# Optimization experiments

Hardware: AMD Instinct MI355X
Metric: run time of the kernel (lower is better)

Reference implementation:

```python
import jax, jax.numpy as jnp
import numpy as np

# Fixed module configuration (matches init_kwargs)
B, T, H, W, C = 2, 16, 32, 32, 512
NH, DH = 8, 64          # num_heads, head_dim = C // NH
MLP = 2048
EPS = 1e-6              # flax LayerNorm default epsilon


def _xavier(key, shape):
    fan_in, fan_out = shape[-2], shape[-1]
    lim = np.sqrt(6.0 / (fan_in + fan_out)).astype(np.float32)
    return jax.random.uniform(key, shape, jnp.float32, -lim, lim)


def setup_inputs() -> dict:
    key = jax.random.key(0)
    ks = jax.random.split(key, 8)
    return {
        "x": jax.random.normal(ks[0], (B, T * H * W, C), jnp.float32),
        # per-axis (stacked: 0=time, 1=height, 2=width) attention params
        "ln_scale": jnp.ones((3, C), jnp.float32),
        "ln_bias": jnp.zeros((3, C), jnp.float32),
        "wq": _xavier(ks[1], (3, C, C)), "bq": jnp.zeros((3, C), jnp.float32),
        "wk": _xavier(ks[2], (3, C, C)), "bk": jnp.zeros((3, C), jnp.float32),
        "wv": _xavier(ks[3], (3, C, C)), "bv": jnp.zeros((3, C), jnp.float32),
        "wo": _xavier(ks[4], (3, C, C)), "bo": jnp.zeros((3, C), jnp.float32),
        # final LN + MLP params
        "ln_mlp_scale": jnp.ones((C,), jnp.float32),
        "ln_mlp_bias": jnp.zeros((C,), jnp.float32),
        "w1": _xavier(ks[5], (C, MLP)),
        "b1": jax.random.normal(ks[6], (MLP,), jnp.float32) * 1e-6,
        "w2": _xavier(ks[7], (MLP, C)),
        "b2": jnp.zeros((C,), jnp.float32),
    }


def _ln(x, scale, bias):
    m = jnp.mean(x, axis=-1, keepdims=True)
    v = jnp.var(x, axis=-1, keepdims=True)
    return (x - m) * jax.lax.rsqrt(v + EPS) * scale + bias


def _mha(x, wq, bq, wk, bk, wv, bv, wo, bo):
    # x: [Bf, S, C]; standard flax-style MHA (query scaled by 1/sqrt(head_dim))
    Bf, S, _ = x.shape
    q = (x @ wq + bq).reshape(Bf, S, NH, DH) * (1.0 / np.sqrt(DH).astype(np.float32))
    k = (x @ wk + bk).reshape(Bf, S, NH, DH)
    v = (x @ wv + bv).reshape(Bf, S, NH, DH)
    a = jax.nn.softmax(jnp.einsum('bqhd,bkhd->bhqk', q, k), axis=-1)
    o = jnp.einsum('bhqk,bkhd->bqhd', a, v).reshape(Bf, S, C)
    return o @ wo + bo


def _axial(x5, axis, sc, bi, wq, bq, wk, bk, wv, bv, wo, bo):
    # fold all non-`axis` spatial dims into batch, attend along `axis`
    other = [a for a in (1, 2, 3) if a != axis]
    perm = [0] + other + [axis, 4]
    xp = jnp.transpose(x5, perm)                      # [..., S_axis, C]
    pshape = xp.shape
    x1 = xp.reshape(-1, pshape[-2], C)                # [Bf, S_axis, C]
    y = _mha(_ln(x1, sc, bi), wq, bq, wk, bk, wv, bv, wo, bo) + x1  # pre-LN residual
    y = y.reshape(pshape)
    inv = list(np.argsort(perm))
    return jnp.transpose(y, inv)


def reference(x, ln_scale, ln_bias, wq, bq, wk, bk, wv, bv, wo, bo,
              ln_mlp_scale, ln_mlp_bias, w1, b1, w2, b2):
    x5 = x.reshape(B, T, H, W, C)
    for i, axis in enumerate((1, 2, 3)):  # time, height, width
        x5 = _axial(x5, axis, ln_scale[i], ln_bias[i], wq[i], bq[i],
                    wk[i], bk[i], wv[i], bv[i], wo[i], bo[i])
    xf = x5.reshape(B, T * H * W, C)
    y = _ln(xf, ln_mlp_scale, ln_mlp_bias)
    y = jax.nn.gelu(y @ w1 + b1) @ w2 + b2            # gelu approximate=True (flax default)
    return xf + y
```

## Files before the change

### kernel.cpp

```cpp
#include <hip/hip_runtime.h>
#include <hip/hip_bf16.h>

typedef __attribute__((ext_vector_type(8))) short short8;
typedef __attribute__((ext_vector_type(4))) float f32x4;

static __device__ __forceinline__ short f2bf(float f) {
    union { __hip_bfloat16 h; short s; } u;
    u.h = __float2bfloat16(f);
    return u.s;
}

static __device__ __forceinline__ float gelu_tanh(float v) {
    const float c = 0.7978845608028654f;
    float t = tanhf(c * (v + 0.044715f * v * v * v));
    return 0.5f * v * (1.f + t);
}

static __device__ __forceinline__ void gload16(const void* g, void* l) {
    __builtin_amdgcn_global_load_lds(
        (const __attribute__((address_space(1))) void*)g,
        (__attribute__((address_space(3))) void*)l, 16, 0, 0);
}

__global__ __launch_bounds__(256) void cvt_weights(
    const float* __restrict__ wq, const float* __restrict__ wk,
    const float* __restrict__ wv, const float* __restrict__ wo,
    const float* __restrict__ w1, const float* __restrict__ w2,
    short* __restrict__ wT)
{
    const long NSQ = 12L * 262144;
    long gid = (long)blockIdx.x * 256 + threadIdx.x;
    if (gid < NSQ) {
        int m = (int)(gid >> 18);
        int rem = (int)(gid & 262143);
        int n = rem >> 9, k = rem & 511;
        int a = m >> 2, t = m & 3;
        const float* src = (t == 0) ? wq : (t == 1) ? wk : (t == 2) ? wv : wo;
        wT[gid] = f2bf(src[(long)a * 262144 + (long)k * 512 + n]);
    } else if (gid < NSQ + 1048576) {
        int r = (int)(gid - NSQ);
        int n = r >> 9, k = r & 511;
        wT[gid] = f2bf(w1[(long)k * 2048 + n]);
    } else {
        int r = (int)(gid - NSQ - 1048576);
        int n = r >> 11, k = r & 2047;
        wT[gid] = f2bf(w2[(long)k * 512 + n]);
    }
}

__global__ __launch_bounds__(256) void ln_kernel(
    const float* __restrict__ x, const float* __restrict__ sc,
    const float* __restrict__ bi, short* __restrict__ out)
{
    int row = blockIdx.x * 4 + (threadIdx.x >> 6);
    int lane = threadIdx.x & 63;
    const float* xr = x + (long)row * 512 + lane * 8;
    f32x4 v0 = *(const f32x4*)xr;
    f32x4 v1 = *(const f32x4*)(xr + 4);
    float s = 0.f, ss = 0.f;
#pragma unroll
    for (int i = 0; i < 4; i++) { s += v0[i] + v1[i]; ss += v0[i] * v0[i] + v1[i] * v1[i]; }
#pragma unroll
    for (int m = 1; m < 64; m <<= 1) { s += __shfl_xor(s, m, 64); ss += __shfl_xor(ss, m, 64); }
    float mean = s * (1.f / 512.f);
    float var  = ss * (1.f / 512.f) - mean * mean;
    float rs = rsqrtf(var + 1e-6f);
    f32x4 s0 = *(const f32x4*)(sc + lane * 8);
    f32x4 s1 = *(const f32x4*)(sc + lane * 8 + 4);
    f32x4 b0 = *(const f32x4*)(bi + lane * 8);
    f32x4 b1 = *(const f32x4*)(bi + lane * 8 + 4);
    short8 o;
#pragma unroll
    for (int i = 0; i < 4; i++) o[i]     = f2bf((v0[i] - mean) * rs * s0[i] + b0[i]);
#pragma unroll
    for (int i = 0; i < 4; i++) o[4 + i] = f2bf((v1[i] - mean) * rs * s1[i] + b1[i]);
    *(short8*)(out + (long)row * 512 + lane * 8) = o;
}

template<int EPI>
__global__ __launch_bounds__(256, 2) void gemm_nt(
    const short* __restrict__ A, const short* __restrict__ Bt,
    const float* __restrict__ bias, const float* __restrict__ bias2,
    const float* __restrict__ bias3,
    const float* __restrict__ res, float* __restrict__ outf,
    short* __restrict__ outb, int M, int N, int K, float scale)
{
    __shared__ __align__(16) short AB[2][2][8192];
    const int t = threadIdx.x;
    const int lane = t & 63, wid = t >> 6;
    const int wm = wid >> 1, wn = wid & 1;
    const int m0 = blockIdx.x * 128, n0 = blockIdx.y * 128;

    const short* Ag = A  + (long)m0 * K;
    const short* Bg = Bt + (long)n0 * K;

    f32x4 acc[4][4];
#pragma unroll
    for (int i = 0; i < 4; i++)
#pragma unroll
        for (int j = 0; j < 4; j++) acc[i][j] = (f32x4){0.f, 0.f, 0.f, 0.f};

    const long rowOff = (long)(t >> 3) * K + (t & 7) * 8;
    const int  ldsOff = t * 16;
    char* const lbase = (char*)AB;
    const int NT = K >> 6;

#pragma unroll
    for (int c = 0; c < 4; c++) {
        gload16(Ag + rowOff + (long)c * 32 * K, lbase + c * 4096 + ldsOff);
        gload16(Bg + rowOff + (long)c * 32 * K, lbase + 16384 + c * 4096 + ldsOff);
    }

    int cur = 0;
    for (int tt = 0; tt < NT; ++tt) {
        if (tt + 1 < NT) {
            const short* Asrc = Ag + (tt + 1) * 64 + rowOff;
            const short* Bsrc = Bg + (tt + 1) * 64 + rowOff;
            char* dst = lbase + (cur ^ 1) * 32768;
#pragma unroll
            for (int c = 0; c < 4; c++) {
                gload16(Asrc + (long)c * 32 * K, dst + c * 4096 + ldsOff);
                gload16(Bsrc + (long)c * 32 * K, dst + 16384 + c * 4096 + ldsOff);
            }
            asm volatile("s_waitcnt vmcnt(8)" ::: "memory");
        } else {
            asm volatile("s_waitcnt vmcnt(0)" ::: "memory");
        }
        asm volatile("s_barrier" ::: "memory");

        const char* rb = lbase + cur * 32768;
        const int arow = wm * 64 + (lane & 15);
        const int brow = wn * 64 + (lane & 15);
        const int kb = (lane >> 4) * 16;
#pragma unroll
        for (int ks = 0; ks < 2; ++ks) {
            short8 af[4], bfr[4];
#pragma unroll
            for (int f = 0; f < 4; f++) {
                af[f]  = *(short8*)(rb + (arow + f * 16) * 128 + kb + ks * 64);
                bfr[f] = *(short8*)(rb + 16384 + (brow + f * 16) * 128 + kb + ks * 64);
            }
#pragma unroll
            for (int i = 0; i < 4; i++)
#pragma unroll
                for (int j = 0; j < 4; j++)
                    acc[i][j] = __builtin_amdgcn_mfma_f32_16x16x32_bf16(af[i], bfr[j], acc[i][j], 0, 0, 0);
        }
        asm volatile("s_barrier" ::: "memory");
        cur ^= 1;
    }

    if (EPI == 1) {
#pragma unroll
        for (int j = 0; j < 4; j++) {
            int col = n0 + wn * 64 + j * 16 + (lane & 15);
            float bv = bias[col];
#pragma unroll
            for (int i = 0; i < 4; i++) {
                int row0 = m0 + wm * 64 + i * 16 + ((lane >> 4) << 2);
#pragma unroll
                for (int r = 0; r < 4; r++) {
                    long idx = (long)(row0 + r) * N + col;
                    outf[idx] = acc[i][j][r] + bv + res[idx];
                }
            }
        }
    } else {
        float* sl = (float*)((char*)AB + (wid >> 1) * 32768 + (wid & 1) * 8192);
        const int r0g = m0 + wm * 64;
        const int c0g = n0 + wn * 64;
#pragma unroll
        for (int half = 0; half < 2; ++half) {
#pragma unroll
            for (int jj = 0; jj < 2; ++jj) {
                int j = half * 2 + jj;
                int col = c0g + j * 16 + (lane & 15);
                float bv, sc_part = 1.f;
                if (EPI == 3) {
                    int part = col >> 9;
                    const float* bp = (part == 0) ? bias : (part == 1) ? bias2 : bias3;
                    bv = bp[col & 511];
                    if (part == 0) sc_part = scale;
                } else {
                    bv = bias[col];
                }
#pragma unroll
                for (int i = 0; i < 4; i++)
#pragma unroll
                    for (int r = 0; r < 4; r++) {
                        int rl = i * 16 + ((lane >> 4) << 2) + r;
                        int cl = jj * 16 + (lane & 15);
                        float v = (acc[i][j][r] + bv) * sc_part;
                        if (EPI == 2) v = gelu_tanh(v);
                        sl[(rl * 32 + cl) ^ ((rl & 7) << 2)] = v;
                    }
            }
            __syncthreads();
#pragma unroll
            for (int s = 0; s < 4; s++) {
                int rl = s * 16 + (lane >> 2);
                int fb = rl * 32 + (lane & 3) * 8;
                int sw = (rl & 7) << 2;
                f32x4 lo = *(f32x4*)&sl[fb ^ sw];
                f32x4 hi = *(f32x4*)&sl[(fb + 4) ^ sw];
                short8 o;
#pragma unroll
                for (int e = 0; e < 4; e++) { o[e] = f2bf(lo[e]); o[4 + e] = f2bf(hi[e]); }
                *(short8*)(outb + (long)(r0g + rl) * N + c0g + half * 32 + (lane & 3) * 8) = o;
            }
            if (half == 0) __syncthreads();
        }
    }
}

template<int S, int PASS>
__global__ __launch_bounds__(64) void attn_kernel(
    const short* __restrict__ Q, const short* __restrict__ Kx,
    const short* __restrict__ V, short* __restrict__ O, int ld)
{
    constexpr int MF = S / 16;
    constexpr int SP = 32;
    __shared__ __align__(16) short P_lds[S * SP];
    __shared__ __align__(16) short Vt[64 * SP];

    const int lane = threadIdx.x;
    const int pair = blockIdx.x;
    const int head = pair & 7;
    const int bf = pair >> 3;
    long base; int stride;
    if (PASS == 0)      { base = (long)(bf >> 10) * 16384 + (bf & 1023); stride = 1024; }
    else if (PASS == 1) { int b = bf >> 9, t = (bf >> 5) & 15, w = bf & 31; base = (long)b * 16384 + t * 1024 + w; stride = 32; }
    else                { int b = bf >> 9, t = (bf >> 5) & 15, h = bf & 31; base = (long)b * 16384 + t * 1024 + (h << 5); stride = 1; }
    const int hoff = head * 64;

    if (S == 16) {
        short8 z = {0, 0, 0, 0, 0, 0, 0, 0};
        *(short8*)(P_lds + lane * 8) = z;
#pragma unroll
        for (int i = 0; i < 4; i++) *(short8*)(Vt + lane * 32 + i * 8) = z;
        __syncthreads();
    }

    short8 qf[MF][2], kf[MF][2];
#pragma unroll
    for (int f = 0; f < MF; f++) {
        int r = f * 16 + (lane & 15);
        const short* qp = Q + (base + (long)r * stride) * ld + hoff + ((lane >> 4) * 8);
        qf[f][0] = *(const short8*)qp;
        qf[f][1] = *(const short8*)(qp + 32);
        const short* kp = Kx + (base + (long)r * stride) * ld + hoff + ((lane >> 4) * 8);
        kf[f][0] = *(const short8*)kp;
        kf[f][1] = *(const short8*)(kp + 32);
    }

    short8 vv[4];
    const int vr  = (S == 32) ? (lane & 31) : (lane & 15);
    const int vd0 = (S == 32) ? ((lane >> 5) * 32) : ((lane >> 4) * 16);
    constexpr int NVC = (S == 32) ? 4 : 2;
    {
        const short* vp = V + (base + (long)vr * stride) * ld + hoff + vd0;
#pragma unroll
        for (int c = 0; c < NVC; c++) vv[c] = *(const short8*)(vp + c * 8);
    }
#pragma unroll
    for (int c = 0; c < NVC; c++)
#pragma unroll
        for (int e = 0; e < 8; e++)
            Vt[(vd0 + c * 8 + e) * SP + vr] = vv[c][e];

    f32x4 zero4 = {0.f, 0.f, 0.f, 0.f};
    f32x4 sc[MF][MF];
#pragma unroll
    for (int i = 0; i < MF; i++)
#pragma unroll
        for (int j = 0; j < MF; j++) {
            f32x4 a = __builtin_amdgcn_mfma_f32_16x16x32_bf16(qf[i][0], kf[j][0], zero4, 0, 0, 0);
            sc[i][j] = __builtin_amdgcn_mfma_f32_16x16x32_bf16(qf[i][1], kf[j][1], a, 0, 0, 0);
        }

#pragma unroll
    for (int i = 0; i < MF; i++) {
#pragma unroll
        for (int r = 0; r < 4; r++) {
            float mx = sc[i][0][r];
            if (MF == 2) mx = fmaxf(mx, sc[i][1][r]);
#pragma unroll
            for (int m = 1; m < 16; m <<= 1) mx = fmaxf(mx, __shfl_xor(mx, m, 64));
            float e0 = expf(sc[i][0][r] - mx);
            float e1 = (MF == 2) ? expf(sc[i][1][r] - mx) : 0.f;
            float sum = e0 + e1;
#pragma unroll
            for (int m = 1; m < 16; m <<= 1) sum += __shfl_xor(sum, m, 64);
            float inv = 1.f / sum;
            int row = i * 16 + ((lane >> 4) << 2) + r;
            P_lds[row * SP + (lane & 15)] = f2bf(e0 * inv);
            if (MF == 2) P_lds[row * SP + 16 + (lane & 15)] = f2bf(e1 * inv);
        }
    }
    __syncthreads();

    short8 pa[MF];
#pragma unroll
    for (int f = 0; f < MF; f++)
        pa[f] = *(const short8*)(P_lds + (f * 16 + (lane & 15)) * SP + (lane >> 4) * 8);
    short8 vbf[4];
#pragma unroll
    for (int n = 0; n < 4; n++)
        vbf[n] = *(const short8*)(Vt + (n * 16 + (lane & 15)) * SP + (lane >> 4) * 8);
    f32x4 of[MF][4];
#pragma unroll
    for (int f = 0; f < MF; f++)
#pragma unroll
        for (int n = 0; n < 4; n++)
            of[f][n] = __builtin_amdgcn_mfma_f32_16x16x32_bf16(pa[f], vbf[n], zero4, 0, 0, 0);

#pragma unroll
    for (int f = 0; f < MF; f++) {
        int q0 = f * 16 + ((lane >> 4) << 2);
#pragma unroll
        for (int n = 0; n < 4; n++) {
            int d = n * 16 + (lane & 15);
#pragma unroll
            for (int r = 0; r < 4; r++)
                O[(base + (long)(q0 + r) * stride) * 512 + hoff + d] = f2bf(of[f][n][r]);
        }
    }
}

extern "C" void kernel_launch(void* const* d_in, const int* in_sizes, int n_in,
                              void* d_out, int out_size, void* d_ws, size_t ws_size,
                              hipStream_t stream)
{
    const float* x   = (const float*)d_in[0];
    const float* lns = (const float*)d_in[1];
    const float* lnb = (const float*)d_in[2];
    const float* wq  = (const float*)d_in[3];
    const float* bq  = (const float*)d_in[4];
    const float* wk  = (const float*)d_in[5];
    const float* bk  = (const float*)d_in[6];
    const float* wv  = (const float*)d_in[7];
    const float* bv  = (const float*)d_in[8];
    const float* wo  = (const float*)d_in[9];
    const float* bo  = (const float*)d_in[10];
    const float* lms = (const float*)d_in[11];
    const float* lmb = (const float*)d_in[12];
    const float* w1  = (const float*)d_in[13];
    const float* b1  = (const float*)d_in[14];
    const float* w2  = (const float*)d_in[15];
    const float* b2  = (const float*)d_in[16];

    char* ws = (char*)d_ws;
    short* wT   = (short*)ws;
    short* bufA = (short*)(ws + 10485760);
    short* big  = (short*)(ws + 10485760 + 33554432);
    float* xcur = (float*)d_out;

    const int M = 32768;

    cvt_weights<<<20480, 256, 0, stream>>>(wq, wk, wv, wo, w1, w2, wT);

    for (int p = 0; p < 3; ++p) {
        const float* xin = (p == 0) ? x : xcur;
        ln_kernel<<<8192, 256, 0, stream>>>(xin, lns + p * 512, lnb + p * 512, bufA);
        const short* wqkvT = wT + (long)(p * 4) * 262144;
        const short* woT   = wT + (long)(p * 4 + 3) * 262144;
        gemm_nt<3><<<dim3(256, 12), 256, 0, stream>>>(bufA, wqkvT,
            bq + p * 512, bk + p * 512, bv + p * 512,
            nullptr, nullptr, big, M, 1536, 512, 0.125f);
        const short* qb = big, *kb = big + 512, *vbp = big + 1024;
        if (p == 0)      attn_kernel<16, 0><<<16384, 64, 0, stream>>>(qb, kb, vbp, bufA, 1536);
        else if (p == 1) attn_kernel<32, 1><<<8192, 64, 0, stream>>>(qb, kb, vbp, bufA, 1536);
        else             attn_kernel<32, 2><<<8192, 64, 0, stream>>>(qb, kb, vbp, bufA, 1536);
        gemm_nt<1><<<dim3(256, 4), 256, 0, stream>>>(bufA, woT,
            bo + p * 512, nullptr, nullptr, xin, xcur, nullptr, M, 512, 512, 1.f);
    }

    ln_kernel<<<8192, 256, 0, stream>>>(xcur, lms, lmb, bufA);
    const short* w1T = wT + 12L * 262144;
    const short* w2T = wT + 12L * 262144 + 1048576;
    gemm_nt<2><<<dim3(256, 16), 256, 0, stream>>>(bufA, w1T, b1,
        nullptr, nullptr, nullptr, nullptr, big, M, 2048, 512, 1.f);
    gemm_nt<1><<<dim3(256, 4), 256, 0, stream>>>(big, w2T, b2,
        nullptr, nullptr, xcur, xcur, nullptr, M, 512, 2048, 1.f);
}
```

Before: 971.5 us.

## Enlarge GEMM tiles to 256x256 with 512-thread blocks and 8x4 MFMA per wave

The bf16 GEMM moves from 128x128 tiles with 4 waves to 256x256 tiles with 8 waves, each wave computing a 128x64 sub-tile. The goal is to raise arithmetic intensity and cut global and LDS traffic per FLOP. The prefetch wait also changes: the next tile's loads are now fully drained at the end of each iteration instead of waiting with vmcnt(8) before compute. In exchange, LDS per block doubles to 128KB, the block count drops a lot (for example 256 blocks for the N=512 GEMMs), and the 128 fp32 accumulators per thread raise register pressure.

```diff
diff --git a/kernel.cpp b/kernel.cpp
--- a/kernel.cpp
+++ b/kernel.cpp
@@ -78,74 +78,72 @@
 }
 
 template<int EPI>
-__global__ __launch_bounds__(256, 2) void gemm_nt(
+__global__ __launch_bounds__(512, 2) void gemm_nt(
     const short* __restrict__ A, const short* __restrict__ Bt,
     const float* __restrict__ bias, const float* __restrict__ bias2,
     const float* __restrict__ bias3,
     const float* __restrict__ res, float* __restrict__ outf,
     short* __restrict__ outb, int M, int N, int K, float scale)
 {
-    __shared__ __align__(16) short AB[2][2][8192];
+    __shared__ __align__(16) char LDS[2][65536];
     const int t = threadIdx.x;
     const int lane = t & 63, wid = t >> 6;
-    const int wm = wid >> 1, wn = wid & 1;
-    const int m0 = blockIdx.x * 128, n0 = blockIdx.y * 128;
+    const int wm = wid >> 2, wn = wid & 3;
+    const int m0 = blockIdx.x * 256, n0 = blockIdx.y * 256;
 
     const short* Ag = A  + (long)m0 * K;
     const short* Bg = Bt + (long)n0 * K;
 
-    f32x4 acc[4][4];
-#pragma unroll
-    for (int i = 0; i < 4; i++)
+    f32x4 acc[8][4];
+#pragma unroll
+    for (int i = 0; i < 8; i++)
 #pragma unroll
         for (int j = 0; j < 4; j++) acc[i][j] = (f32x4){0.f, 0.f, 0.f, 0.f};
 
     const long rowOff = (long)(t >> 3) * K + (t & 7) * 8;
     const int  ldsOff = t * 16;
-    char* const lbase = (char*)AB;
     const int NT = K >> 6;
 
 #pragma unroll
     for (int c = 0; c < 4; c++) {
-        gload16(Ag + rowOff + (long)c * 32 * K, lbase + c * 4096 + ldsOff);
-        gload16(Bg + rowOff + (long)c * 32 * K, lbase + 16384 + c * 4096 + ldsOff);
-    }
+        gload16(Ag + rowOff + (long)c * 64 * K, LDS[0] + c * 8192 + ldsOff);
+        gload16(Bg + rowOff + (long)c * 64 * K, LDS[0] + 32768 + c * 8192 + ldsOff);
+    }
+    asm volatile("s_waitcnt vmcnt(0)" ::: "memory");
+    asm volatile("s_barrier" ::: "memory");
 
     int cur = 0;
     for (int tt = 0; tt < NT; ++tt) {
         if (tt + 1 < NT) {
             const short* Asrc = Ag + (tt + 1) * 64 + rowOff;
             const short* Bsrc = Bg + (tt + 1) * 64 + rowOff;
-            char* dst = lbase + (cur ^ 1) * 32768;
+            char* dst = LDS[cur ^ 1];
 #pragma unroll
             for (int c = 0; c < 4; c++) {
-                gload16(Asrc + (long)c * 32 * K, dst + c * 4096 + ldsOff);
-                gload16(Bsrc + (long)c * 32 * K, dst + 16384 + c * 4096 + ldsOff);
+                gload16(Asrc + (long)c * 64 * K, dst + c * 8192 + ldsOff);
+                gload16(Bsrc + (long)c * 64 * K, dst + 32768 + c * 8192 + ldsOff);
             }
-            asm volatile("s_waitcnt vmcnt(8)" ::: "memory");
-        } else {
-            asm volatile("s_waitcnt vmcnt(0)" ::: "memory");
-        }
-        asm volatile("s_barrier" ::: "memory");
-
-        const char* rb = lbase + cur * 32768;
-        const int arow = wm * 64 + (lane & 15);
+        }
+        const char* rb = LDS[cur];
+        const int arow = wm * 128 + (lane & 15);
         const int brow = wn * 64 + (lane & 15);
         const int kb = (lane >> 4) * 16;
 #pragma unroll
         for (int ks = 0; ks < 2; ++ks) {
-            short8 af[4], bfr[4];
-#pragma unroll
-            for (int f = 0; f < 4; f++) {
-                af[f]  = *(short8*)(rb + (arow + f * 16) * 128 + kb + ks * 64);
-                bfr[f] = *(short8*)(rb + 16384 + (brow + f * 16) * 128 + kb + ks * 64);
-            }
-#pragma unroll
-            for (int i = 0; i < 4; i++)
-#pragma unroll
-                for (int j = 0; j < 4; j++)
-                    acc[i][j] = __builtin_amdgcn_mfma_f32_16x16x32_bf16(af[i], bfr[j], acc[i][j], 0, 0, 0);
-        }
+            short8 af[8], bfr[4];
+#pragma unroll
+            for (int mf = 0; mf < 8; mf++)
+                af[mf] = *(const short8*)(rb + (arow + mf * 16) * 128 + kb + ks * 64);
+#pragma unroll
+            for (int n = 0; n < 4; n++)
+                bfr[n] = *(const short8*)(rb + 32768 + (brow + n * 16) * 128 + kb + ks * 64);
+#pragma unroll
+            for (int mf = 0; mf < 8; mf++)
+#pragma unroll
+                for (int n = 0; n < 4; n++)
+                    acc[mf][n] = __builtin_amdgcn_mfma_f32_16x16x32_bf16(af[mf], bfr[n], acc[mf][n], 0, 0, 0);
+        }
+        asm volatile("s_waitcnt vmcnt(0)" ::: "memory");
         asm volatile("s_barrier" ::: "memory");
         cur ^= 1;
     }
@@ -156,8 +154,8 @@
             int col = n0 + wn * 64 + j * 16 + (lane & 15);
             float bv = bias[col];
 #pragma unroll
-            for (int i = 0; i < 4; i++) {
-                int row0 = m0 + wm * 64 + i * 16 + ((lane >> 4) << 2);
+            for (int i = 0; i < 8; i++) {
+                int row0 = m0 + wm * 128 + i * 16 + ((lane >> 4) << 2);
 #pragma unroll
                 for (int r = 0; r < 4; r++) {
                     long idx = (long)(row0 + r) * N + col;
@@ -166,49 +164,52 @@
             }
         }
     } else {
-        float* sl = (float*)((char*)AB + (wid >> 1) * 32768 + (wid & 1) * 8192);
-        const int r0g = m0 + wm * 64;
+        float* sl = (float*)((char*)LDS + wid * 8192);
         const int c0g = n0 + wn * 64;
 #pragma unroll
-        for (int half = 0; half < 2; ++half) {
-#pragma unroll
-            for (int jj = 0; jj < 2; ++jj) {
-                int j = half * 2 + jj;
-                int col = c0g + j * 16 + (lane & 15);
-                float bv, sc_part = 1.f;
-                if (EPI == 3) {
-                    int part = col >> 9;
-                    const float* bp = (part == 0) ? bias : (part == 1) ? bias2 : bias3;
-                    bv = bp[col & 511];
-                    if (part == 0) sc_part = scale;
-                } else {
-                    bv = bias[col];
+        for (int mb = 0; mb < 2; ++mb) {
+            const int r0g = m0 + wm * 128 + mb * 64;
+#pragma unroll
+            for (int half = 0; half < 2; ++half) {
+#pragma unroll
+                for (int jj = 0; jj < 2; ++jj) {
+                    int j = half * 2 + jj;
+                    int col = c0g + j * 16 + (lane & 15);
+                    float bv, sc_part = 1.f;
+                    if (EPI == 3) {
+                        int part = col >> 9;
+                        const float* bp = (part == 0) ? bias : (part == 1) ? bias2 : bias3;
+                        bv = bp[col & 511];
+                        if (part == 0) sc_part = scale;
+                    } else {
+                        bv = bias[col];
+                    }
+#pragma unroll
+                    for (int i = 0; i < 4; i++)
+#pragma unroll
+                        for (int r = 0; r < 4; r++) {
+                            int rl = i * 16 + ((lane >> 4) << 2) + r;
+                            int cl = jj * 16 + (lane & 15);
+                            float v = (acc[mb * 4 + i][j] [r] + bv) * sc_part;
+                            if (EPI == 2) v = gelu_tanh(v);
+                            sl[(rl * 32 + cl) ^ ((rl & 7) << 2)] = v;
+                        }
                 }
-#pragma unroll
-                for (int i = 0; i < 4; i++)
-#pragma unroll
-                    for (int r = 0; r < 4; r++) {
-                        int rl = i * 16 + ((lane >> 4) << 2) + r;
-                        int cl = jj * 16 + (lane & 15);
-                        float v = (acc[i][j][r] + bv) * sc_part;
-                        if (EPI == 2) v = gelu_tanh(v);
-                        sl[(rl * 32 + cl) ^ ((rl & 7) << 2)] = v;
-                    }
+                __syncthreads();
+#pragma unroll
+                for (int s = 0; s < 4; s++) {
+                    int rl = s * 16 + (lane >> 2);
+                    int fb = rl * 32 + (lane & 3) * 8;
+                    int sw = (rl & 7) << 2;
+                    f32x4 lo = *(f32x4*)&sl[fb ^ sw];
+                    f32x4 hi = *(f32x4*)&sl[(fb + 4) ^ sw];
+                    short8 o;
+#pragma unroll
+                    for (int e = 0; e < 4; e++) { o[e] = f2bf(lo[e]); o[4 + e] = f2bf(hi[e]); }
+                    *(short8*)(outb + (long)(r0g + rl) * N + c0g + half * 32 + (lane & 3) * 8) = o;
+                }
+                __syncthreads();
             }
-            __syncthreads();
-#pragma unroll
-            for (int s = 0; s < 4; s++) {
-                int rl = s * 16 + (lane >> 2);
-                int fb = rl * 32 + (lane & 3) * 8;
-                int sw = (rl & 7) << 2;
-                f32x4 lo = *(f32x4*)&sl[fb ^ sw];
-                f32x4 hi = *(f32x4*)&sl[(fb + 4) ^ sw];
-                short8 o;
-#pragma unroll
-                for (int e = 0; e < 4; e++) { o[e] = f2bf(lo[e]); o[4 + e] = f2bf(hi[e]); }
-                *(short8*)(outb + (long)(r0g + rl) * N + c0g + half * 32 + (lane & 3) * 8) = o;
-            }
-            if (half == 0) __syncthreads();
         }
     }
 }
@@ -364,22 +365,22 @@
         ln_kernel<<<8192, 256, 0, stream>>>(xin, lns + p * 512, lnb + p * 512, bufA);
         const short* wqkvT = wT + (long)(p * 4) * 262144;
         const short* woT   = wT + (long)(p * 4 + 3) * 262144;
-        gemm_nt<3><<<dim3(256, 12), 256, 0, stream>>>(bufA, wqkvT,
+        gemm_nt<3><<<dim3(128, 6), 512, 0, stream>>>(bufA, wqkvT,
             bq + p * 512, bk + p * 512, bv + p * 512,
             nullptr, nullptr, big, M, 1536, 512, 0.125f);
         const short* qb = big, *kb = big + 512, *vbp = big + 1024;
         if (p == 0)      attn_kernel<16, 0><<<16384, 64, 0, stream>>>(qb, kb, vbp, bufA, 1536);
         else if (p == 1) attn_kernel<32, 1><<<8192, 64, 0, stream>>>(qb, kb, vbp, bufA, 1536);
         else             attn_kernel<32, 2><<<8192, 64, 0, stream>>>(qb, kb, vbp, bufA, 1536);
-        gemm_nt<1><<<dim3(256, 4), 256, 0, stream>>>(bufA, woT,
+        gemm_nt<1><<<dim3(128, 2), 512, 0, stream>>>(bufA, woT,
             bo + p * 512, nullptr, nullptr, xin, xcur, nullptr, M, 512, 512, 1.f);
     }
 
     ln_kernel<<<8192, 256, 0, stream>>>(xcur, lms, lmb, bufA);
     const short* w1T = wT + 12L * 262144;
     const short* w2T = wT + 12L * 262144 + 1048576;
-    gemm_nt<2><<<dim3(256, 16), 256, 0, stream>>>(bufA, w1T, b1,
+    gemm_nt<2><<<dim3(128, 8), 512, 0, stream>>>(bufA, w1T, b1,
         nullptr, nullptr, nullptr, nullptr, big, M, 2048, 512, 1.f);
-    gemm_nt<1><<<dim3(256, 4), 256, 0, stream>>>(big, w2T, b2,
+    gemm_nt<1><<<dim3(128, 2), 512, 0, stream>>>(big, w2T, b2,
         nullptr, nullptr, xcur, xcur, nullptr, M, 512, 2048, 1.f);
 }
```

Result: no change. 954.7 us (-1.7%).
